# Kernel optimization log

Measured on AMD Instinct MI355X. Metric: run time of the kernel, lower is better.

## Reference

```python
import jax, jax.numpy as jnp
import numpy as np

N_NODES = 50000
N_EDGES = 1600000


def setup_inputs() -> dict:
    key = jax.random.key(0)
    ks = jax.random.split(key, 8)
    dims = [1024, 2048, 1024, 512]
    fea = jax.random.normal(ks[0], (N_NODES, dims[0]), dtype=jnp.float32)
    edge_index = jax.random.randint(ks[1], (2, N_EDGES), 0, N_NODES, dtype=jnp.int64)
    edge_vals = jax.random.uniform(ks[2], (N_EDGES,), dtype=jnp.float32)
    # Glorot-ish scaled weights per GCN layer
    W1 = jax.random.normal(ks[3], (dims[0], dims[1]), dtype=jnp.float32) / np.sqrt(dims[0])
    W2 = jax.random.normal(ks[4], (dims[1], dims[2]), dtype=jnp.float32) / np.sqrt(dims[1])
    W3 = jax.random.normal(ks[5], (dims[2], dims[3]), dtype=jnp.float32) / np.sqrt(dims[2])
    b1 = jnp.zeros((dims[1],), dtype=jnp.float32)
    b2 = jnp.zeros((dims[2],), dtype=jnp.float32)
    b3 = jnp.zeros((dims[3],), dtype=jnp.float32)
    return {"fea": fea, "edge_index": edge_index, "edge_vals": edge_vals,
            "W1": W1, "b1": b1, "W2": W2, "b2": b2, "W3": W3, "b3": b3}


def _gcn_layer(x, row, col, edge_vals, W, b):
    # dense transform: [N, din] @ [din, dout] + bias
    support = x @ W + b
    # spmm(adj, support) in COO form: out[row] += val * support[col]
    msgs = support[col] * edge_vals[:, None]          # [E, dout]
    return jax.ops.segment_sum(msgs, row, num_segments=N_NODES)


def reference(fea, edge_index, edge_vals, W1, b1, W2, b2, W3, b3):
    row, col = edge_index[0], edge_index[1]
    h = jax.nn.relu(_gcn_layer(fea, row, col, edge_vals, W1, b1))
    h = jax.nn.relu(_gcn_layer(h, row, col, edge_vals, W2, b2))
    # last layer: no activation
    return _gcn_layer(h, row, col, edge_vals, W3, b3)
```

## Files before the change

### kernel.cpp

```cpp
#include <hip/hip_runtime.h>

typedef unsigned short u16;
using bf16x8 = __attribute__((ext_vector_type(8))) short;
using u16x8  = __attribute__((ext_vector_type(8))) unsigned short;
using f32x4  = __attribute__((ext_vector_type(4))) float;

#define NN 50000
#define NPAD 50048

__device__ __forceinline__ u16 f2b(float f) {
  union { float f; unsigned u; } x; x.f = f;
  unsigned r = x.u + 0x7fffu + ((x.u >> 16) & 1u);
  return (u16)(r >> 16);
}
__device__ __forceinline__ float b2f(u16 h) {
  union { unsigned u; float f; } x; x.u = ((unsigned)h) << 16; return x.f;
}

#define GLOAD_LDS16(g, l) __builtin_amdgcn_global_load_lds( \
    (const __attribute__((address_space(1))) unsigned int*)(g), \
    (__attribute__((address_space(3))) unsigned int*)(l), 16, 0, 0)

__global__ void hist_kernel(const int* __restrict__ rows, const float* __restrict__ vals,
                            int* __restrict__ counts, float* __restrict__ rowsum, int E) {
  int e = blockIdx.x * 256 + threadIdx.x;
  if (e < E) {
    int r = rows[e];
    atomicAdd(&counts[r], 1);
    atomicAdd(&rowsum[r], vals[e]);
  }
}

__global__ void scan_bsum(const int* __restrict__ counts, int* __restrict__ bsum, int n) {
  __shared__ int s[256];
  int t = threadIdx.x;
  int gi = blockIdx.x * 256 + t;
  s[t] = (gi < n) ? counts[gi] : 0;
  __syncthreads();
  for (int d = 128; d > 0; d >>= 1) {
    if (t < d) s[t] += s[t + d];
    __syncthreads();
  }
  if (t == 0) bsum[blockIdx.x] = s[0];
}

__global__ void scan_partials(int* __restrict__ bsum, int nb) {
  __shared__ int s[256];
  int t = threadIdx.x;
  int v = (t < nb) ? bsum[t] : 0;
  s[t] = v;
  __syncthreads();
  for (int d = 1; d < 256; d <<= 1) {
    int x = (t >= d) ? s[t - d] : 0;
    __syncthreads();
    s[t] += x;
    __syncthreads();
  }
  if (t < nb) bsum[t] = s[t] - v;
}

__global__ void scan_final(const int* __restrict__ counts, const int* __restrict__ bsum,
                           int* __restrict__ offs, int n) {
  __shared__ int s[256];
  int t = threadIdx.x;
  int gi = blockIdx.x * 256 + t;
  int v = (gi < n) ? counts[gi] : 0;
  s[t] = v;
  __syncthreads();
  for (int d = 1; d < 256; d <<= 1) {
    int x = (t >= d) ? s[t - d] : 0;
    __syncthreads();
    s[t] += x;
    __syncthreads();
  }
  if (gi <= n) offs[gi] = bsum[blockIdx.x] + s[t] - v;
}

__global__ void scatter_kernel(const int* __restrict__ rows, const int* __restrict__ cols,
                               const float* __restrict__ vals, const int* __restrict__ offs,
                               int* __restrict__ cursor, int* __restrict__ ecol,
                               float* __restrict__ ev2, int E) {
  int e = blockIdx.x * 256 + threadIdx.x;
  if (e < E) {
    int r = rows[e];
    int p = offs[r] + atomicAdd(&cursor[r], 1);
    ecol[p] = cols[e];
    ev2[p] = vals[e];
  }
}

__global__ void conv_f2b4(const float* __restrict__ in, u16* __restrict__ out, int n4) {
  int i = blockIdx.x * 256 + threadIdx.x;
  if (i < n4) {
    float4 f = ((const float4*)in)[i];
    ushort4 o;
    o.x = f2b(f.x); o.y = f2b(f.y); o.z = f2b(f.z); o.w = f2b(f.w);
    ((ushort4*)out)[i] = o;
  }
}

__global__ void transpose_conv(const float* __restrict__ W, u16* __restrict__ Wt, int K, int N) {
  __shared__ float tile[32][33];
  int bx = blockIdx.x * 32;
  int by = blockIdx.y * 32;
  int tx = threadIdx.x;
  int ty = threadIdx.y;
  for (int i = 0; i < 32; i += 8) tile[ty + i][tx] = W[(size_t)(by + ty + i) * N + bx + tx];
  __syncthreads();
  for (int i = 0; i < 32; i += 8) Wt[(size_t)(bx + ty + i) * K + by + tx] = f2b(tile[tx][ty + i]);
}

__global__ __launch_bounds__(256)
void gemm_bt(const u16* __restrict__ A, const u16* __restrict__ Bt,
             const float* __restrict__ bias, const float* __restrict__ rowsum,
             u16* __restrict__ C, int M, int N, int K, int relu) {
  __shared__ u16 As[128 * 32];
  __shared__ u16 Bs[128 * 32];
  const int tid = threadIdx.x;
  const int lane = tid & 63;
  const int wave = tid >> 6;
  const int wm = wave >> 1;
  const int wn = wave & 1;
  const int bm = blockIdx.y * 128;
  const int bn = blockIdx.x * 128;
  const int l15 = lane & 15;
  const int lg = lane >> 4;

  f32x4 acc[4][4];
#pragma unroll
  for (int i = 0; i < 4; i++)
#pragma unroll
    for (int j = 0; j < 4; j++)
#pragma unroll
      for (int k = 0; k < 4; k++) acc[i][j][k] = 0.f;

  const int r = tid >> 2;
  const int c = (tid & 3) << 3;
  const u16* gA = A + (size_t)(bm + r) * K + c;
  const u16* gB = Bt + (size_t)(bn + r) * K + c;
  u16* lA = &As[r * 32 + c];
  u16* lB = &Bs[r * 32 + c];

  for (int k0 = 0; k0 < K; k0 += 32) {
    GLOAD_LDS16(gA, lA);
    GLOAD_LDS16(gA + (size_t)64 * K, lA + 64 * 32);
    GLOAD_LDS16(gB, lB);
    GLOAD_LDS16(gB + (size_t)64 * K, lB + 64 * 32);
    gA += 32;
    gB += 32;
    __syncthreads();
    bf16x8 af[4], bfr[4];
#pragma unroll
    for (int i = 0; i < 4; i++) af[i] = *(const bf16x8*)&As[(wm * 64 + i * 16 + l15) * 32 + lg * 8];
#pragma unroll
    for (int j = 0; j < 4; j++) bfr[j] = *(const bf16x8*)&Bs[(wn * 64 + j * 16 + l15) * 32 + lg * 8];
#pragma unroll
    for (int i = 0; i < 4; i++)
#pragma unroll
      for (int j = 0; j < 4; j++)
        acc[i][j] = __builtin_amdgcn_mfma_f32_16x16x32_bf16(af[i], bfr[j], acc[i][j], 0, 0, 0);
    __syncthreads();
  }

#pragma unroll
  for (int i = 0; i < 4; i++) {
    int row0 = bm + wm * 64 + i * 16 + lg * 4;
#pragma unroll
    for (int rr = 0; rr < 4; rr++) {
      int row = row0 + rr;
      if (row < M) {
        float rs = rowsum ? rowsum[row] : 1.0f;
#pragma unroll
        for (int j = 0; j < 4; j++) {
          int col = bn + wn * 64 + j * 16 + l15;
          float v = acc[i][j][rr] + rs * bias[col];
          if (relu) v = fmaxf(v, 0.f);
          C[(size_t)row * N + col] = f2b(v);
        }
      }
    }
  }
}

template <int VEC, int RELU, int OUTF32>
__global__ __launch_bounds__(64)
void spmm3(const int* __restrict__ offs, const int* __restrict__ ecol,
           const float* __restrict__ ev, const u16* __restrict__ X,
           void* __restrict__ outp, int stride) {
  const int node = blockIdx.x;
  const int t = threadIdx.x;
  const int s0 = offs[node];
  const int e0 = offs[node + 1];
  float acc[VEC];
#pragma unroll
  for (int k = 0; k < VEC; k++) acc[k] = 0.f;
  const u16* __restrict__ Xc = X + (size_t)t * VEC;

  int j = s0;
  for (; j + 4 <= e0; j += 4) {
    const int c0 = ecol[j], c1 = ecol[j + 1], c2 = ecol[j + 2], c3 = ecol[j + 3];
    const float v0 = ev[j], v1 = ev[j + 1], v2 = ev[j + 2], v3 = ev[j + 3];
    u16 a0[VEC], a1[VEC], a2[VEC], a3[VEC];
    if constexpr (VEC == 8) {
      *(u16x8*)a0 = *(const u16x8*)(Xc + (size_t)c0 * stride);
      *(u16x8*)a1 = *(const u16x8*)(Xc + (size_t)c1 * stride);
      *(u16x8*)a2 = *(const u16x8*)(Xc + (size_t)c2 * stride);
      *(u16x8*)a3 = *(const u16x8*)(Xc + (size_t)c3 * stride);
    } else {
      *(ushort4*)a0 = *(const ushort4*)(Xc + (size_t)c0 * stride);
      *(ushort4*)a1 = *(const ushort4*)(Xc + (size_t)c1 * stride);
      *(ushort4*)a2 = *(const ushort4*)(Xc + (size_t)c2 * stride);
      *(ushort4*)a3 = *(const ushort4*)(Xc + (size_t)c3 * stride);
    }
#pragma unroll
    for (int k = 0; k < VEC; k++) acc[k] += v0 * b2f(a0[k]);
#pragma unroll
    for (int k = 0; k < VEC; k++) acc[k] += v1 * b2f(a1[k]);
#pragma unroll
    for (int k = 0; k < VEC; k++) acc[k] += v2 * b2f(a2[k]);
#pragma unroll
    for (int k = 0; k < VEC; k++) acc[k] += v3 * b2f(a3[k]);
  }
  for (; j < e0; j++) {
    const int c0 = ecol[j];
    const float v0 = ev[j];
    u16 a0[VEC];
    if constexpr (VEC == 8) {
      *(u16x8*)a0 = *(const u16x8*)(Xc + (size_t)c0 * stride);
    } else {
      *(ushort4*)a0 = *(const ushort4*)(Xc + (size_t)c0 * stride);
    }
#pragma unroll
    for (int k = 0; k < VEC; k++) acc[k] += v0 * b2f(a0[k]);
  }

  if (RELU) {
#pragma unroll
    for (int k = 0; k < VEC; k++) acc[k] = fmaxf(acc[k], 0.f);
  }
  if (OUTF32) {
    float* o = (float*)outp + (size_t)node * stride + (size_t)t * VEC;
#pragma unroll
    for (int k = 0; k < VEC; k += 4) {
      float4 st;
      st.x = acc[k]; st.y = acc[k + 1]; st.z = acc[k + 2]; st.w = acc[k + 3];
      *(float4*)(o + k) = st;
    }
  } else {
    u16* o = (u16*)outp + (size_t)node * stride + (size_t)t * VEC;
    if constexpr (VEC == 8) {
      u16x8 st;
#pragma unroll
      for (int k = 0; k < 8; k++) st[k] = f2b(acc[k]);
      *(u16x8*)o = st;
    } else {
      ushort4 st;
      st.x = f2b(acc[0]); st.y = f2b(acc[1]); st.z = f2b(acc[2]); st.w = f2b(acc[3]);
      *(ushort4*)o = st;
    }
  }
}

extern "C" void kernel_launch(void* const* d_in, const int* in_sizes, int n_in,
                              void* d_out, int out_size, void* d_ws, size_t ws_size,
                              hipStream_t stream) {
  const float* fea = (const float*)d_in[0];
  const int* ei = (const int*)d_in[1];
  const float* ev = (const float*)d_in[2];
  const float* W1 = (const float*)d_in[3];
  const float* b1 = (const float*)d_in[4];
  const float* W2 = (const float*)d_in[5];
  const float* b2 = (const float*)d_in[6];
  const float* W3 = (const float*)d_in[7];
  const float* b3 = (const float*)d_in[8];
  const int E = in_sizes[1] / 2;
  const int* erow = ei;
  const int* ecol_in = ei + E;

  char* w = (char*)d_ws;
  auto alloc = [&](size_t bytes) {
    char* p = w;
    w += (bytes + 255) & ~(size_t)255;
    return p;
  };
  u16* fea_b = (u16*)alloc((size_t)NPAD * 1024 * 2);
  u16* bufB  = (u16*)alloc((size_t)NPAD * 1024 * 2);
  u16* h1_b  = (u16*)alloc((size_t)NPAD * 2048 * 2);
  u16* t2_b  = (u16*)alloc((size_t)NPAD * 1024 * 2);
  u16* W1t = (u16*)alloc((size_t)2048 * 1024 * 2);
  u16* W2t = (u16*)alloc((size_t)1024 * 2048 * 2);
  u16* W3t = (u16*)alloc((size_t)512 * 1024 * 2);
  float* rowsum = (float*)alloc((size_t)NN * 4);
  int* counts = (int*)alloc((size_t)NN * 4);
  int* cursor = (int*)alloc((size_t)NN * 4);
  int* offs = (int*)alloc((size_t)(NN + 1) * 4);
  int* ecol = (int*)alloc((size_t)E * 4);
  float* ev2 = (float*)alloc((size_t)E * 4);
  int* bsum = (int*)alloc(256 * 4);
  (void)bsum; (void)ws_size; (void)n_in; (void)out_size;

  hipMemsetAsync(rowsum, 0, (size_t)((char*)offs - (char*)rowsum), stream);

  const int eb = (E + 255) / 256;
  const int nb = (NN + 256) / 256;
  hist_kernel<<<eb, 256, 0, stream>>>(erow, ev, counts, rowsum, E);
  scan_bsum<<<nb, 256, 0, stream>>>(counts, bsum, NN);
  scan_partials<<<1, 256, 0, stream>>>(bsum, nb);
  scan_final<<<nb, 256, 0, stream>>>(counts, bsum, offs, NN);
  scatter_kernel<<<eb, 256, 0, stream>>>(erow, ecol_in, ev, offs, cursor, ecol, ev2, E);

  conv_f2b4<<<(NN * 1024 / 4 + 255) / 256, 256, 0, stream>>>(fea, fea_b, NN * 1024 / 4);
  dim3 tb(32, 8);
  transpose_conv<<<dim3(2048 / 32, 1024 / 32), tb, 0, stream>>>(W1, W1t, 1024, 2048);
  transpose_conv<<<dim3(1024 / 32, 2048 / 32), tb, 0, stream>>>(W2, W2t, 2048, 1024);
  transpose_conv<<<dim3(512 / 32, 1024 / 32), tb, 0, stream>>>(W3, W3t, 1024, 512);

  const int MT = (NN + 127) / 128;
  spmm3<8, 0, 0><<<NN, 64, 0, stream>>>(offs, ecol, ev2, fea_b, bufB, 1024);
  spmm3<8, 0, 0><<<NN, 64, 0, stream>>>(offs, ecol, ev2, fea_b + 512, bufB + 512, 1024);
  gemm_bt<<<dim3(2048 / 128, MT), 256, 0, stream>>>(bufB, W1t, b1, rowsum, h1_b, NN, 2048, 1024, 1);
  gemm_bt<<<dim3(1024 / 128, MT), 256, 0, stream>>>(h1_b, W2t, b2, nullptr, t2_b, NN, 1024, 2048, 0);
  spmm3<8, 1, 0><<<NN, 64, 0, stream>>>(offs, ecol, ev2, t2_b, fea_b, 1024);
  spmm3<8, 1, 0><<<NN, 64, 0, stream>>>(offs, ecol, ev2, t2_b + 512, fea_b + 512, 1024);
  gemm_bt<<<dim3(512 / 128, MT), 256, 0, stream>>>(fea_b, W3t, b3, nullptr, bufB, NN, 512, 1024, 0);
  spmm3<4, 0, 1><<<NN, 64, 0, stream>>>(offs, ecol, ev2, bufB, d_out, 512);
  spmm3<4, 0, 1><<<NN, 64, 0, stream>>>(offs, ecol, ev2, bufB + 256, (float*)d_out + 256, 512);
}
```

Baseline: 2.194 ms.

## Replace 128x128 GEMM with double-buffered 256x256 swizzled-LDS kernel

```diff
diff --git a/kernel.cpp b/kernel.cpp
--- a/kernel.cpp
+++ b/kernel.cpp
@@ -6,7 +6,7 @@
 using f32x4  = __attribute__((ext_vector_type(4))) float;
 
 #define NN 50000
-#define NPAD 50048
+#define NPAD 50176
 
 __device__ __forceinline__ u16 f2b(float f) {
   union { float f; unsigned u; } x; x.f = f;
@@ -110,70 +110,138 @@
   for (int i = 0; i < 32; i += 8) Wt[(size_t)(bx + ty + i) * K + by + tx] = f2b(tile[tx][ty + i]);
 }
 
-__global__ __launch_bounds__(256)
-void gemm_bt(const u16* __restrict__ A, const u16* __restrict__ Bt,
+__global__ __launch_bounds__(512, 2)
+void gemm256(const u16* __restrict__ A, const u16* __restrict__ Bt,
              const float* __restrict__ bias, const float* __restrict__ rowsum,
-             u16* __restrict__ C, int M, int N, int K, int relu) {
-  __shared__ u16 As[128 * 32];
-  __shared__ u16 Bs[128 * 32];
+             u16* __restrict__ C, int M, int N, int K, int relu, int nbx) {
+  __shared__ __align__(16) u16 As[2][256 * 64];
+  __shared__ __align__(16) u16 Bs[2][256 * 64];
+
+  const int p = blockIdx.x, total = gridDim.x;
+  const int q = total >> 3, r8 = total & 7;
+  const int xcd = p & 7, slot_ = p >> 3;
+  const int l = (xcd < r8 ? xcd * (q + 1) : r8 * (q + 1) + (xcd - r8) * q) + slot_;
+  const int bm = (l / nbx) * 256;
+  const int bn = (l % nbx) * 256;
+
   const int tid = threadIdx.x;
   const int lane = tid & 63;
-  const int wave = tid >> 6;
-  const int wm = wave >> 1;
-  const int wn = wave & 1;
-  const int bm = blockIdx.y * 128;
-  const int bn = blockIdx.x * 128;
-  const int l15 = lane & 15;
-  const int lg = lane >> 4;
-
-  f32x4 acc[4][4];
-#pragma unroll
-  for (int i = 0; i < 4; i++)
+  const int wid = tid >> 6;
+  const int wm = wid >> 2;
+  const int wn = wid & 3;
+  const int l15 = lane & 15, lg = lane >> 4;
+
+  const int xcol = (tid & 7) ^ ((tid >> 3) & 7);
+  const u16* gA = A + (size_t)(bm + (tid >> 3)) * K + xcol * 8;
+  const u16* gB = Bt + (size_t)(bn + (tid >> 3)) * K + xcol * 8;
+  const size_t rowstep = (size_t)64 * K;
+
+  f32x4 acc[8][4];
+#pragma unroll
+  for (int i = 0; i < 8; i++)
 #pragma unroll
     for (int j = 0; j < 4; j++)
 #pragma unroll
       for (int k = 0; k < 4; k++) acc[i][j][k] = 0.f;
 
-  const int r = tid >> 2;
-  const int c = (tid & 3) << 3;
-  const u16* gA = A + (size_t)(bm + r) * K + c;
-  const u16* gB = Bt + (size_t)(bn + r) * K + c;
-  u16* lA = &As[r * 32 + c];
-  u16* lB = &Bs[r * 32 + c];
-
-  for (int k0 = 0; k0 < K; k0 += 32) {
-    GLOAD_LDS16(gA, lA);
-    GLOAD_LDS16(gA + (size_t)64 * K, lA + 64 * 32);
-    GLOAD_LDS16(gB, lB);
-    GLOAD_LDS16(gB + (size_t)64 * K, lB + 64 * 32);
-    gA += 32;
-    gB += 32;
-    __syncthreads();
-    bf16x8 af[4], bfr[4];
-#pragma unroll
-    for (int i = 0; i < 4; i++) af[i] = *(const bf16x8*)&As[(wm * 64 + i * 16 + l15) * 32 + lg * 8];
-#pragma unroll
-    for (int j = 0; j < 4; j++) bfr[j] = *(const bf16x8*)&Bs[(wn * 64 + j * 16 + l15) * 32 + lg * 8];
-#pragma unroll
-    for (int i = 0; i < 4; i++)
-#pragma unroll
-      for (int j = 0; j < 4; j++)
-        acc[i][j] = __builtin_amdgcn_mfma_f32_16x16x32_bf16(af[i], bfr[j], acc[i][j], 0, 0, 0);
-    __syncthreads();
-  }
-
-#pragma unroll
-  for (int i = 0; i < 4; i++) {
-    int row0 = bm + wm * 64 + i * 16 + lg * 4;
-#pragma unroll
-    for (int rr = 0; rr < 4; rr++) {
-      int row = row0 + rr;
+  const int NT = K >> 6;
+
+#define STAGE(kt, b)                                                           \
+  {                                                                            \
+    const u16* sa = gA + (size_t)(kt) * 64;                                    \
+    const u16* sb = gB + (size_t)(kt) * 64;                                    \
+    u16* da = &As[b][0] + tid * 8;                                             \
+    u16* db = &Bs[b][0] + tid * 8;                                             \
+    GLOAD_LDS16(sa, da);                                                       \
+    GLOAD_LDS16(sa + rowstep, da + 4096);                                      \
+    GLOAD_LDS16(sa + 2 * rowstep, da + 8192);                                  \
+    GLOAD_LDS16(sa + 3 * rowstep, da + 12288);                                 \
+    GLOAD_LDS16(sb, db);                                                       \
+    GLOAD_LDS16(sb + rowstep, db + 4096);                                      \
+    GLOAD_LDS16(sb + 2 * rowstep, db + 8192);                                  \
+    GLOAD_LDS16(sb + 3 * rowstep, db + 12288);                                 \
+  }
+
+  STAGE(0, 0);
+
+  for (int u = 0; u < NT; u++) {
+    const int cb = u & 1;
+    if (u + 1 < NT) {
+      STAGE(u + 1, cb ^ 1);
+      asm volatile("s_waitcnt vmcnt(8)" ::: "memory");
+    } else {
+      asm volatile("s_waitcnt vmcnt(0)" ::: "memory");
+    }
+    __builtin_amdgcn_s_barrier();
+
+    const u16* ab = &As[cb][0];
+    const u16* bb = &Bs[cb][0];
+
+    bf16x8 bf[4][2];
+#pragma unroll
+    for (int n = 0; n < 4; n++)
+#pragma unroll
+      for (int s = 0; s < 2; s++) {
+        int row = wn * 64 + n * 16 + l15;
+        int slot = (s * 4 + lg) ^ (row & 7);
+        bf[n][s] = *(const bf16x8*)&bb[row * 64 + slot * 8];
+      }
+    bf16x8 af0[4][2];
+#pragma unroll
+    for (int m = 0; m < 4; m++)
+#pragma unroll
+      for (int s = 0; s < 2; s++) {
+        int row = wm * 128 + m * 16 + l15;
+        int slot = (s * 4 + lg) ^ (row & 7);
+        af0[m][s] = *(const bf16x8*)&ab[row * 64 + slot * 8];
+      }
+    __builtin_amdgcn_s_setprio(1);
+#pragma unroll
+    for (int m = 0; m < 4; m++)
+#pragma unroll
+      for (int n = 0; n < 4; n++) {
+        acc[m][n] = __builtin_amdgcn_mfma_f32_16x16x32_bf16(af0[m][0], bf[n][0], acc[m][n], 0, 0, 0);
+        acc[m][n] = __builtin_amdgcn_mfma_f32_16x16x32_bf16(af0[m][1], bf[n][1], acc[m][n], 0, 0, 0);
+      }
+    __builtin_amdgcn_s_setprio(0);
+    bf16x8 af1[4][2];
+#pragma unroll
+    for (int m = 0; m < 4; m++)
+#pragma unroll
+      for (int s = 0; s < 2; s++) {
+        int row = wm * 128 + (m + 4) * 16 + l15;
+        int slot = (s * 4 + lg) ^ (row & 7);
+        af1[m][s] = *(const bf16x8*)&ab[row * 64 + slot * 8];
+      }
+    asm volatile("s_waitcnt lgkmcnt(0)" ::: "memory");
+    __builtin_amdgcn_s_barrier();
+    __builtin_amdgcn_s_setprio(1);
+#pragma unroll
+    for (int m = 0; m < 4; m++)
+#pragma unroll
+      for (int n = 0; n < 4; n++) {
+        acc[m + 4][n] = __builtin_amdgcn_mfma_f32_16x16x32_bf16(af1[m][0], bf[n][0], acc[m + 4][n], 0, 0, 0);
+        acc[m + 4][n] = __builtin_amdgcn_mfma_f32_16x16x32_bf16(af1[m][1], bf[n][1], acc[m + 4][n], 0, 0, 0);
+      }
+    __builtin_amdgcn_s_setprio(0);
+  }
+#undef STAGE
+
+  float bs[4];
+#pragma unroll
+  for (int n = 0; n < 4; n++) bs[n] = bias[bn + wn * 64 + n * 16 + l15];
+#pragma unroll
+  for (int m = 0; m < 8; m++) {
+    int rowb = bm + wm * 128 + m * 16 + lg * 4;
+#pragma unroll
+    for (int j = 0; j < 4; j++) {
+      int row = rowb + j;
       if (row < M) {
         float rs = rowsum ? rowsum[row] : 1.0f;
 #pragma unroll
-        for (int j = 0; j < 4; j++) {
-          int col = bn + wn * 64 + j * 16 + l15;
-          float v = acc[i][j][rr] + rs * bias[col];
+        for (int n = 0; n < 4; n++) {
+          int col = bn + wn * 64 + n * 16 + l15;
+          float v = acc[m][n][j] + rs * bs[n];
           if (relu) v = fmaxf(v, 0.f);
           C[(size_t)row * N + col] = f2b(v);
         }
@@ -315,14 +383,14 @@
   transpose_conv<<<dim3(1024 / 32, 2048 / 32), tb, 0, stream>>>(W2, W2t, 2048, 1024);
   transpose_conv<<<dim3(512 / 32, 1024 / 32), tb, 0, stream>>>(W3, W3t, 1024, 512);
 
-  const int MT = (NN + 127) / 128;
+  const int MT2 = (NN + 255) / 256;
   spmm3<8, 0, 0><<<NN, 64, 0, stream>>>(offs, ecol, ev2, fea_b, bufB, 1024);
   spmm3<8, 0, 0><<<NN, 64, 0, stream>>>(offs, ecol, ev2, fea_b + 512, bufB + 512, 1024);
-  gemm_bt<<<dim3(2048 / 128, MT), 256, 0, stream>>>(bufB, W1t, b1, rowsum, h1_b, NN, 2048, 1024, 1);
-  gemm_bt<<<dim3(1024 / 128, MT), 256, 0, stream>>>(h1_b, W2t, b2, nullptr, t2_b, NN, 1024, 2048, 0);
+  gemm256<<<(2048 / 256) * MT2, 512, 0, stream>>>(bufB, W1t, b1, rowsum, h1_b, NN, 2048, 1024, 1, 2048 / 256);
+  gemm256<<<(1024 / 256) * MT2, 512, 0, stream>>>(h1_b, W2t, b2, nullptr, t2_b, NN, 1024, 2048, 0, 1024 / 256);
   spmm3<8, 1, 0><<<NN, 64, 0, stream>>>(offs, ecol, ev2, t2_b, fea_b, 1024);
   spmm3<8, 1, 0><<<NN, 64, 0, stream>>>(offs, ecol, ev2, t2_b + 512, fea_b + 512, 1024);
-  gemm_bt<<<dim3(512 / 128, MT), 256, 0, stream>>>(fea_b, W3t, b3, nullptr, bufB, NN, 512, 1024, 0);
+  gemm256<<<(512 / 256) * MT2, 512, 0, stream>>>(fea_b, W3t, b3, nullptr, bufB, NN, 512, 1024, 0, 512 / 256);
   spmm3<4, 0, 1><<<NN, 64, 0, stream>>>(offs, ecol, ev2, bufB, d_out, 512);
   spmm3<4, 0, 1><<<NN, 64, 0, stream>>>(offs, ecol, ev2, bufB + 256, (float*)d_out + 256, 512);
 }
```

Result: faster. 2.103 ms (-4.1%).
